# Kernel tuning notes

Hardware: AMD Instinct MI355X
Metric: run time of the kernel (lower is better)

The kernel has to match this reference:

```python
import jax, jax.numpy as jnp
import numpy as np

N_NODES = 100000
N_EDGES = 3200000
IN_DIM, HIDDEN, OUT_DIM = 512, 128, 64


def setup_inputs() -> dict:
    key = jax.random.key(0)
    ks = jax.random.split(key, 6)
    features = jax.random.normal(ks[0], (N_NODES, IN_DIM), dtype=jnp.float32)
    W1 = jax.random.normal(ks[1], (IN_DIM, HIDDEN), dtype=jnp.float32) * (1.0 / np.sqrt(IN_DIM))
    W2 = jax.random.normal(ks[2], (HIDDEN, OUT_DIM), dtype=jnp.float32) * (1.0 / np.sqrt(HIDDEN))
    edge_weight = jax.random.uniform(ks[3], (N_EDGES,), dtype=jnp.float32)
    edge_src = jax.random.randint(ks[4], (N_EDGES,), 0, N_NODES, dtype=jnp.int32)
    edge_dst = jax.random.randint(ks[5], (N_EDGES,), 0, N_NODES, dtype=jnp.int32)
    return {"features": features, "W1": W1, "W2": W2,
            "edge_weight": edge_weight, "edge_src": edge_src, "edge_dst": edge_dst}


def _propagate(h, edge_weight, edge_src, edge_dst):
    # z = A @ h, A given as COO edge list. Equivalent to the chunked spmm:
    # Graph_output[j] = sum_i adj_chunk[i][j] @ feature_chunk[i]
    msgs = edge_weight[:, None] * h[edge_src]          # [E, D]
    return jax.ops.segment_sum(msgs, edge_dst, num_segments=N_NODES)


def reference(features, W1, W2, edge_weight, edge_src, edge_dst):
    # NN layers: mm + relu between layers, no relu after last (nlayers=2)
    h = jax.nn.relu(features @ W1)
    h = h @ W2
    # Graph propagation applied nlayers (=2) times; the feature-dim padding
    # in the torch code is a no-op on the math (stripped after the loop).
    h = _propagate(h, edge_weight, edge_src, edge_dst)
    h = _propagate(h, edge_weight, edge_src, edge_dst)
    return h
```

## Files before the change

### kernel.cpp

```cpp
#include <hip/hip_runtime.h>

#define NN    100000
#define IND   512
#define HID   128
#define OUTD  64
#define NBUCK 782
#define NB    256
#define NGEMM 782
#define NPREP 64

typedef _Float16 half8_t __attribute__((ext_vector_type(8)));
typedef _Float16 half4_t __attribute__((ext_vector_type(4)));
typedef float f32x4 __attribute__((ext_vector_type(4)));

__global__ __launch_bounds__(1024) void countprep_k(const int* __restrict__ dst,
                                                    int* __restrict__ counts, int nE, int CH,
                                                    const float* __restrict__ W1,
                                                    const float* __restrict__ W2,
                                                    _Float16* __restrict__ W1t,
                                                    _Float16* __restrict__ W2t) {
    __shared__ int bins[NBUCK];
    const int bid = blockIdx.x, tid = threadIdx.x;
    if (bid >= NB) {
        int idx = (bid - NB) * 1024 + tid;
        if (idx < IND * HID) { int c = idx >> 9, k = idx & 511; W1t[idx] = (_Float16)W1[k * HID + c]; }
        if (idx < HID * OUTD) { int c = idx >> 7, k = idx & 127; W2t[idx] = (_Float16)W2[k * OUTD + c]; }
        return;
    }
    for (int b = tid; b < NBUCK; b += 1024) bins[b] = 0;
    __syncthreads();
    int lo = bid * CH, hi = min(lo + CH, nE);
    for (int e = lo + tid; e < hi; e += 1024) atomicAdd(&bins[dst[e] >> 7], 1);
    __syncthreads();
    for (int b = tid; b < NBUCK; b += 1024) counts[b * NB + bid] = bins[b];
}

__global__ __launch_bounds__(256) void bsum_k(const int* __restrict__ counts,
                                              int* __restrict__ bsum) {
    __shared__ int s[256];
    const int b = blockIdx.x, t = threadIdx.x;
    s[t] = counts[b * NB + t];
    __syncthreads();
    for (int off = 128; off > 0; off >>= 1) {
        if (t < off) s[t] += s[t + off];
        __syncthreads();
    }
    if (t == 0) bsum[b] = s[0];
}

__global__ __launch_bounds__(1024) void scan_top_k(const int* __restrict__ bsum,
                                                   int* __restrict__ bucketStart, int n) {
    __shared__ int s[1024];
    const int t = threadIdx.x;
    int v = (t < n) ? bsum[t] : 0;
    s[t] = v;
    __syncthreads();
    for (int off = 1; off < 1024; off <<= 1) {
        int x = (t >= off) ? s[t - off] : 0;
        __syncthreads();
        s[t] += x;
        __syncthreads();
    }
    if (t < n) bucketStart[t] = s[t] - v;
    if (t == n - 1) bucketStart[n] = s[t];
}

__global__ __launch_bounds__(256) void boff_k(int* __restrict__ counts,
                                              const int* __restrict__ bucketStart) {
    __shared__ int s[256];
    const int b = blockIdx.x, t = threadIdx.x;
    int v = counts[b * NB + t];
    s[t] = v;
    __syncthreads();
    for (int off = 1; off < 256; off <<= 1) {
        int x = (t >= off) ? s[t - off] : 0;
        __syncthreads();
        s[t] += x;
        __syncthreads();
    }
    counts[b * NB + t] = bucketStart[b] + s[t] - v;
}

__global__ __launch_bounds__(1024) void part_k(const int* __restrict__ src,
                                               const int* __restrict__ dst,
                                               const float* __restrict__ ew,
                                               const int* __restrict__ offsets,
                                               unsigned* __restrict__ edata, int nE, int CH) {
    __shared__ int cur[NBUCK];
    const int j = blockIdx.x, tid = threadIdx.x;
    for (int b = tid; b < NBUCK; b += 1024) cur[b] = offsets[b * NB + j];
    __syncthreads();
    int lo = j * CH, hi = min(lo + CH, nE);
    for (int e = lo + tid; e < hi; e += 1024) {
        int d = dst[e];
        int b = d >> 7;
        int pos = atomicAdd(&cur[b], 1);
        int q = (int)(ew[e] * 255.f + 0.5f);
        if (q > 255) q = 255;
        edata[pos] = ((unsigned)(d & 127) << 25) | ((unsigned)src[e] << 8) | (unsigned)q;
    }
}

__global__ __launch_bounds__(256) void gemmsort_k(const float* __restrict__ F,
                                                  const _Float16* __restrict__ W1t,
                                                  const _Float16* __restrict__ W2t,
                                                  _Float16* __restrict__ H2,
                                                  const unsigned* __restrict__ edata,
                                                  const int* __restrict__ bucketStart,
                                                  unsigned* __restrict__ epack,
                                                  int* __restrict__ rowStart) {
    __shared__ _Float16 smem[128 * 64 * 2];
    __shared__ _Float16 W2s[64 * 128];
    const int tid = threadIdx.x;

    if (blockIdx.x < NBUCK) {
        int* bins = (int*)smem;
        int* s    = bins + 128;
        int* cur  = bins + 256;
        const int b = blockIdx.x;
        if (tid < 128) bins[tid] = 0;
        __syncthreads();
        const int beg = bucketStart[b], end = bucketStart[b + 1];
        for (int e = beg + tid; e < end; e += 256)
            atomicAdd(&bins[edata[e] >> 25], 1);
        __syncthreads();
        if (tid < 128) s[tid] = bins[tid];
        __syncthreads();
        for (int off = 1; off < 128; off <<= 1) {
            int x = 0;
            if (tid < 128 && tid >= off) x = s[tid - off];
            __syncthreads();
            if (tid < 128) s[tid] += x;
            __syncthreads();
        }
        if (tid < 128) {
            int excl = beg + s[tid] - bins[tid];
            cur[tid] = excl;
            rowStart[b * 128 + tid] = excl;
        }
        __syncthreads();
        for (int e = beg + tid; e < end; e += 256) {
            unsigned r = edata[e];
            int ld = r >> 25;
            int pos = atomicAdd(&cur[ld], 1);
            epack[pos] = r & 0x1FFFFFFu;
        }
        return;
    }

    _Float16* At = smem;
    _Float16* Bt = smem + 128 * 64;
    const int wid  = tid >> 6;
    const int lane = tid & 63;
    const int l15  = lane & 15;
    const int l4   = lane >> 4;
    const int brow = (blockIdx.x - NBUCK) * 128;

#pragma unroll
    for (int i = 0; i < 4; i++) {
        int idx = i * 256 + tid;
        int r = idx >> 4, sl = idx & 15;
        int u = (r * 128 + sl * 8) ^ ((r & 7) << 3);
        *(uint4*)(&W2s[u]) = *(const uint4*)(W2t + r * 128 + sl * 8);
    }

    f32x4 acc[2][8];
#pragma unroll
    for (int mt = 0; mt < 2; mt++)
#pragma unroll
        for (int nt = 0; nt < 8; nt++) acc[mt][nt] = (f32x4)0.f;

    for (int chunk = 0; chunk < 8; chunk++) {
        const int kc = chunk * 64;
#pragma unroll
        for (int i = 0; i < 8; i++) {
            int idx = i * 256 + tid;
            int r = idx >> 4, c4 = idx & 15;
            int gr = brow + r; if (gr >= NN) gr = NN - 1;
            float4 v = *(const float4*)(F + (size_t)gr * IND + kc + c4 * 4);
            half4_t h; h.x = (_Float16)v.x; h.y = (_Float16)v.y; h.z = (_Float16)v.z; h.w = (_Float16)v.w;
            int u = (r * 64 + c4 * 4) ^ ((r & 7) << 3);
            *(half4_t*)(&At[u]) = h;
        }
#pragma unroll
        for (int i = 0; i < 4; i++) {
            int idx = i * 256 + tid;
            int r = idx >> 3, sl = idx & 7;
            int u = (r * 64 + sl * 8) ^ ((r & 7) << 3);
            *(uint4*)(&Bt[u]) = *(const uint4*)(W1t + (size_t)r * IND + kc + sl * 8);
        }
        __syncthreads();
#pragma unroll
        for (int kk = 0; kk < 2; kk++) {
            const int kc2 = kk * 32;
            half8_t af[2];
#pragma unroll
            for (int mt = 0; mt < 2; mt++) {
                int rloc = wid * 32 + mt * 16 + l15;
                int u = (rloc * 64 + kc2 + l4 * 8) ^ ((rloc & 7) << 3);
                af[mt] = *(half8_t*)(&At[u]);
            }
#pragma unroll
            for (int nt = 0; nt < 8; nt++) {
                int cloc = nt * 16 + l15;
                int u = (cloc * 64 + kc2 + l4 * 8) ^ ((cloc & 7) << 3);
                half8_t bf = *(half8_t*)(&Bt[u]);
                acc[0][nt] = __builtin_amdgcn_mfma_f32_16x16x32_f16(af[0], bf, acc[0][nt], 0, 0, 0);
                acc[1][nt] = __builtin_amdgcn_mfma_f32_16x16x32_f16(af[1], bf, acc[1][nt], 0, 0, 0);
            }
        }
        __syncthreads();
    }

    _Float16* H1w = smem + wid * (32 * 128);
#pragma unroll
    for (int mt = 0; mt < 2; mt++)
#pragma unroll
        for (int nt = 0; nt < 8; nt++)
#pragma unroll
            for (int r = 0; r < 4; r++) {
                int rloc = mt * 16 + l4 * 4 + r;
                int col  = nt * 16 + l15;
                float v = acc[mt][nt][r];
                v = v > 0.f ? v : 0.f;
                int u = (rloc * 128 + col) ^ ((rloc & 7) << 3);
                H1w[u] = (_Float16)v;
            }

    f32x4 acc2[2][4];
#pragma unroll
    for (int mt = 0; mt < 2; mt++)
#pragma unroll
        for (int nt = 0; nt < 4; nt++) acc2[mt][nt] = (f32x4)0.f;

#pragma unroll
    for (int kk = 0; kk < 4; kk++) {
        const int kc = kk * 32;
        half8_t a2[2];
#pragma unroll
        for (int mt = 0; mt < 2; mt++) {
            int rloc = mt * 16 + l15;
            int u = (rloc * 128 + kc + l4 * 8) ^ ((rloc & 7) << 3);
            a2[mt] = *(half8_t*)(&H1w[u]);
        }
#pragma unroll
        for (int nt = 0; nt < 4; nt++) {
            int c = nt * 16 + l15;
            int u = (c * 128 + kc + l4 * 8) ^ ((c & 7) << 3);
            half8_t b2 = *(half8_t*)(&W2s[u]);
            acc2[0][nt] = __builtin_amdgcn_mfma_f32_16x16x32_f16(a2[0], b2, acc2[0][nt], 0, 0, 0);
            acc2[1][nt] = __builtin_amdgcn_mfma_f32_16x16x32_f16(a2[1], b2, acc2[1][nt], 0, 0, 0);
        }
    }
#pragma unroll
    for (int mt = 0; mt < 2; mt++)
#pragma unroll
        for (int nt = 0; nt < 4; nt++)
#pragma unroll
            for (int r = 0; r < 4; r++) {
                int grow = brow + wid * 32 + mt * 16 + l4 * 4 + r;
                if (grow < NN) H2[(size_t)grow * OUTD + nt * 16 + l15] = (_Float16)acc2[mt][nt][r];
            }
}

template <bool LAST>
__global__ __launch_bounds__(256) void pull_k(const _Float16* __restrict__ H,
                                              const unsigned* __restrict__ ep,
                                              const int* __restrict__ rowStart,
                                              _Float16* __restrict__ Zh,
                                              float* __restrict__ Zf) {
    int wv = (int)((blockIdx.x * (long)blockDim.x + threadIdx.x) >> 6);
    const int row = __builtin_amdgcn_readfirstlane(wv);
    const int lane = threadIdx.x & 63;
    if (row >= NN) return;
    const int beg = rowStart[row];
    const int end = rowStart[row + 1];
    float acc = 0.f;
    int i = beg;
    for (; i + 8 <= end; i += 8) {
        unsigned u0 = ep[i],     u1 = ep[i + 1], u2 = ep[i + 2], u3 = ep[i + 3];
        unsigned u4 = ep[i + 4], u5 = ep[i + 5], u6 = ep[i + 6], u7 = ep[i + 7];
        float h0 = (float)H[(size_t)(u0 >> 8) * OUTD + lane];
        float h1 = (float)H[(size_t)(u1 >> 8) * OUTD + lane];
        float h2 = (float)H[(size_t)(u2 >> 8) * OUTD + lane];
        float h3 = (float)H[(size_t)(u3 >> 8) * OUTD + lane];
        float h4 = (float)H[(size_t)(u4 >> 8) * OUTD + lane];
        float h5 = (float)H[(size_t)(u5 >> 8) * OUTD + lane];
        float h6 = (float)H[(size_t)(u6 >> 8) * OUTD + lane];
        float h7 = (float)H[(size_t)(u7 >> 8) * OUTD + lane];
        acc += (float)(int)(u0 & 255u) * h0;
        acc += (float)(int)(u1 & 255u) * h1;
        acc += (float)(int)(u2 & 255u) * h2;
        acc += (float)(int)(u3 & 255u) * h3;
        acc += (float)(int)(u4 & 255u) * h4;
        acc += (float)(int)(u5 & 255u) * h5;
        acc += (float)(int)(u6 & 255u) * h6;
        acc += (float)(int)(u7 & 255u) * h7;
    }
    for (; i + 4 <= end; i += 4) {
        unsigned u0 = ep[i], u1 = ep[i + 1], u2 = ep[i + 2], u3 = ep[i + 3];
        float h0 = (float)H[(size_t)(u0 >> 8) * OUTD + lane];
        float h1 = (float)H[(size_t)(u1 >> 8) * OUTD + lane];
        float h2 = (float)H[(size_t)(u2 >> 8) * OUTD + lane];
        float h3 = (float)H[(size_t)(u3 >> 8) * OUTD + lane];
        acc += (float)(int)(u0 & 255u) * h0;
        acc += (float)(int)(u1 & 255u) * h1;
        acc += (float)(int)(u2 & 255u) * h2;
        acc += (float)(int)(u3 & 255u) * h3;
    }
    for (; i < end; i++) {
        unsigned u = ep[i];
        acc += (float)(int)(u & 255u) * (float)H[(size_t)(u >> 8) * OUTD + lane];
    }
    acc *= (1.f / 255.f);
    if (LAST) Zf[(size_t)row * OUTD + lane] = acc;
    else      Zh[(size_t)row * OUTD + lane] = (_Float16)acc;
}

extern "C" void kernel_launch(void* const* d_in, const int* in_sizes, int n_in,
                              void* d_out, int out_size, void* d_ws, size_t ws_size,
                              hipStream_t stream) {
    const float* F   = (const float*)d_in[0];
    const float* W1  = (const float*)d_in[1];
    const float* W2  = (const float*)d_in[2];
    const float* ew  = (const float*)d_in[3];
    const int*   src = (const int*)d_in[4];
    const int*   dst = (const int*)d_in[5];
    float* out = (float*)d_out;
    const int nE = in_sizes[3];

    char* p = (char*)d_ws;
    _Float16*  h2        = (_Float16*)p;  p += (size_t)NN * OUTD * sizeof(_Float16);
    _Float16*  z1        = (_Float16*)p;  p += (size_t)NN * OUTD * sizeof(_Float16);
    _Float16*  W1t       = (_Float16*)p;  p += (size_t)HID * IND * sizeof(_Float16);
    _Float16*  W2t       = (_Float16*)p;  p += (size_t)OUTD * HID * sizeof(_Float16);
    int*       counts    = (int*)p;       p += (size_t)NBUCK * NB * sizeof(int);
    int*       bsum      = (int*)p;       p += (size_t)NBUCK * sizeof(int);
    int*       bucketStart=(int*)p;       p += (size_t)(NBUCK + 16) * sizeof(int);
    int*       rowStart  = (int*)p;       p += (size_t)(NN + 160) * sizeof(int);
    unsigned*  edata     = (unsigned*)p;  p += (size_t)nE * sizeof(unsigned);
    unsigned*  epack     = (unsigned*)p;  p += (size_t)nE * sizeof(unsigned);

    const int CH = (nE + NB - 1) / NB;

    countprep_k<<<NB + NPREP, 1024, 0, stream>>>(dst, counts, nE, CH, W1, W2, W1t, W2t);
    bsum_k<<<NBUCK, 256, 0, stream>>>(counts, bsum);
    scan_top_k<<<1, 1024, 0, stream>>>(bsum, bucketStart, NBUCK);
    boff_k<<<NBUCK, 256, 0, stream>>>(counts, bucketStart);
    part_k<<<NB, 1024, 0, stream>>>(src, dst, ew, counts, edata, nE, CH);

    gemmsort_k<<<NBUCK + NGEMM, 256, 0, stream>>>(F, W1t, W2t, h2,
                                                  edata, bucketStart, epack, rowStart);

    int blocks = (int)(((long)NN * 64 + 255) / 256);
    pull_k<false><<<blocks, 256, 0, stream>>>(h2, epack, rowStart, z1, nullptr);
    pull_k<true><<<blocks, 256, 0, stream>>>(z1, epack, rowStart, nullptr, out);
}
```

Baseline: 255.2 us.

## Split GEMM tiles across partition and sort kernels to overlap work

Moves the GEMM into a device function and splits its 782 tiles into two halves. One half now runs in the same launch as the edge partition step, which is now 256-thread blocks, and the other half runs alongside the per-bucket sort. The aim is to hide the latency-bound partition and sort phases behind compute-bound GEMM tiles instead of running partition alone. The risks are more shared-memory pressure on the partition blocks, which now also hold the GEMM buffers, and 4x fewer threads per partition block.

```diff
diff --git a/kernel.cpp b/kernel.cpp
--- a/kernel.cpp
+++ b/kernel.cpp
@@ -7,6 +7,8 @@
 #define NBUCK 782
 #define NB    256
 #define NGEMM 782
+#define GH1   392
+#define GH2   390
 #define NPREP 64
 
 typedef _Float16 half8_t __attribute__((ext_vector_type(8)));
@@ -81,80 +83,18 @@
     counts[b * NB + t] = bucketStart[b] + s[t] - v;
 }
 
-__global__ __launch_bounds__(1024) void part_k(const int* __restrict__ src,
-                                               const int* __restrict__ dst,
-                                               const float* __restrict__ ew,
-                                               const int* __restrict__ offsets,
-                                               unsigned* __restrict__ edata, int nE, int CH) {
-    __shared__ int cur[NBUCK];
-    const int j = blockIdx.x, tid = threadIdx.x;
-    for (int b = tid; b < NBUCK; b += 1024) cur[b] = offsets[b * NB + j];
-    __syncthreads();
-    int lo = j * CH, hi = min(lo + CH, nE);
-    for (int e = lo + tid; e < hi; e += 1024) {
-        int d = dst[e];
-        int b = d >> 7;
-        int pos = atomicAdd(&cur[b], 1);
-        int q = (int)(ew[e] * 255.f + 0.5f);
-        if (q > 255) q = 255;
-        edata[pos] = ((unsigned)(d & 127) << 25) | ((unsigned)src[e] << 8) | (unsigned)q;
-    }
-}
-
-__global__ __launch_bounds__(256) void gemmsort_k(const float* __restrict__ F,
-                                                  const _Float16* __restrict__ W1t,
-                                                  const _Float16* __restrict__ W2t,
-                                                  _Float16* __restrict__ H2,
-                                                  const unsigned* __restrict__ edata,
-                                                  const int* __restrict__ bucketStart,
-                                                  unsigned* __restrict__ epack,
-                                                  int* __restrict__ rowStart) {
-    __shared__ _Float16 smem[128 * 64 * 2];
-    __shared__ _Float16 W2s[64 * 128];
-    const int tid = threadIdx.x;
-
-    if (blockIdx.x < NBUCK) {
-        int* bins = (int*)smem;
-        int* s    = bins + 128;
-        int* cur  = bins + 256;
-        const int b = blockIdx.x;
-        if (tid < 128) bins[tid] = 0;
-        __syncthreads();
-        const int beg = bucketStart[b], end = bucketStart[b + 1];
-        for (int e = beg + tid; e < end; e += 256)
-            atomicAdd(&bins[edata[e] >> 25], 1);
-        __syncthreads();
-        if (tid < 128) s[tid] = bins[tid];
-        __syncthreads();
-        for (int off = 1; off < 128; off <<= 1) {
-            int x = 0;
-            if (tid < 128 && tid >= off) x = s[tid - off];
-            __syncthreads();
-            if (tid < 128) s[tid] += x;
-            __syncthreads();
-        }
-        if (tid < 128) {
-            int excl = beg + s[tid] - bins[tid];
-            cur[tid] = excl;
-            rowStart[b * 128 + tid] = excl;
-        }
-        __syncthreads();
-        for (int e = beg + tid; e < end; e += 256) {
-            unsigned r = edata[e];
-            int ld = r >> 25;
-            int pos = atomicAdd(&cur[ld], 1);
-            epack[pos] = r & 0x1FFFFFFu;
-        }
-        return;
-    }
-
+__device__ __forceinline__ void gemm_tile(int tile, const float* __restrict__ F,
+                                          const _Float16* __restrict__ W1t,
+                                          const _Float16* __restrict__ W2t,
+                                          _Float16* __restrict__ H2,
+                                          _Float16* smem, _Float16* W2s, int tid) {
     _Float16* At = smem;
     _Float16* Bt = smem + 128 * 64;
     const int wid  = tid >> 6;
     const int lane = tid & 63;
     const int l15  = lane & 15;
     const int l4   = lane >> 4;
-    const int brow = (blockIdx.x - NBUCK) * 128;
+    const int brow = tile * 128;
 
 #pragma unroll
     for (int i = 0; i < 4; i++) {
@@ -261,6 +201,87 @@
                 int grow = brow + wid * 32 + mt * 16 + l4 * 4 + r;
                 if (grow < NN) H2[(size_t)grow * OUTD + nt * 16 + l15] = (_Float16)acc2[mt][nt][r];
             }
+}
+
+__global__ __launch_bounds__(256) void partgemm_k(const int* __restrict__ src,
+                                                  const int* __restrict__ dst,
+                                                  const float* __restrict__ ew,
+                                                  const int* __restrict__ offsets,
+                                                  unsigned* __restrict__ edata, int nE, int CH,
+                                                  const float* __restrict__ F,
+                                                  const _Float16* __restrict__ W1t,
+                                                  const _Float16* __restrict__ W2t,
+                                                  _Float16* __restrict__ H2) {
+    __shared__ _Float16 smem[128 * 64 * 2];
+    __shared__ _Float16 W2s[64 * 128];
+    const int tid = threadIdx.x;
+
+    if (blockIdx.x < NB) {
+        int* cur = (int*)smem;
+        const int j = blockIdx.x;
+        for (int b = tid; b < NBUCK; b += 256) cur[b] = offsets[b * NB + j];
+        __syncthreads();
+        int lo = j * CH, hi = min(lo + CH, nE);
+        for (int e = lo + tid; e < hi; e += 256) {
+            int d = dst[e];
+            int b = d >> 7;
+            int pos = atomicAdd(&cur[b], 1);
+            int q = (int)(ew[e] * 255.f + 0.5f);
+            if (q > 255) q = 255;
+            edata[pos] = ((unsigned)(d & 127) << 25) | ((unsigned)src[e] << 8) | (unsigned)q;
+        }
+        return;
+    }
+    gemm_tile(blockIdx.x - NB, F, W1t, W2t, H2, smem, W2s, tid);
+}
+
+__global__ __launch_bounds__(256) void sortgemm_k(const unsigned* __restrict__ edata,
+                                                  const int* __restrict__ bucketStart,
+                                                  unsigned* __restrict__ epack,
+                                                  int* __restrict__ rowStart,
+                                                  const float* __restrict__ F,
+                                                  const _Float16* __restrict__ W1t,
+                                                  const _Float16* __restrict__ W2t,
+                                                  _Float16* __restrict__ H2) {
+    __shared__ _Float16 smem[128 * 64 * 2];
+    __shared__ _Float16 W2s[64 * 128];
+    const int tid = threadIdx.x;
+
+    if (blockIdx.x < NBUCK) {
+        int* bins = (int*)smem;
+        int* s    = bins + 128;
+        int* cur  = bins + 256;
+        const int b = blockIdx.x;
+        if (tid < 128) bins[tid] = 0;
+        __syncthreads();
+        const int beg = bucketStart[b], end = bucketStart[b + 1];
+        for (int e = beg + tid; e < end; e += 256)
+            atomicAdd(&bins[edata[e] >> 25], 1);
+        __syncthreads();
+        if (tid < 128) s[tid] = bins[tid];
+        __syncthreads();
+        for (int off = 1; off < 128; off <<= 1) {
+            int x = 0;
+            if (tid < 128 && tid >= off) x = s[tid - off];
+            __syncthreads();
+            if (tid < 128) s[tid] += x;
+            __syncthreads();
+        }
+        if (tid < 128) {
+            int excl = beg + s[tid] - bins[tid];
+            cur[tid] = excl;
+            rowStart[b * 128 + tid] = excl;
+        }
+        __syncthreads();
+        for (int e = beg + tid; e < end; e += 256) {
+            unsigned r = edata[e];
+            int ld = r >> 25;
+            int pos = atomicAdd(&cur[ld], 1);
+            epack[pos] = r & 0x1FFFFFFu;
+        }
+        return;
+    }
+    gemm_tile(blockIdx.x - NBUCK + GH1, F, W1t, W2t, H2, smem, W2s, tid);
 }
 
 template <bool LAST>
@@ -347,10 +368,11 @@
     bsum_k<<<NBUCK, 256, 0, stream>>>(counts, bsum);
     scan_top_k<<<1, 1024, 0, stream>>>(bsum, bucketStart, NBUCK);
     boff_k<<<NBUCK, 256, 0, stream>>>(counts, bucketStart);
-    part_k<<<NB, 1024, 0, stream>>>(src, dst, ew, counts, edata, nE, CH);
-
-    gemmsort_k<<<NBUCK + NGEMM, 256, 0, stream>>>(F, W1t, W2t, h2,
-                                                  edata, bucketStart, epack, rowStart);
+
+    partgemm_k<<<NB + GH1, 256, 0, stream>>>(src, dst, ew, counts, edata, nE, CH,
+                                             F, W1t, W2t, h2);
+    sortgemm_k<<<NBUCK + GH2, 256, 0, stream>>>(edata, bucketStart, epack, rowStart,
+                                                F, W1t, W2t, h2);
 
     int blocks = (int)(((long)NN * 64 + 255) / 256);
     pull_k<false><<<blocks, 256, 0, stream>>>(h2, epack, rowStart, z1, nullptr);
```

Result: slower. 272.2 us (+6.7%).
